# Kernel tuning notes

Measured on AMD Instinct MI355X. Metric: run time of the kernel, lower is better.

## Reference

```python
import jax, jax.numpy as jnp
import numpy as np

NUM_GROUPS = 9
POWER_P = 4.0
B = 8192

def setup_inputs() -> dict:
    key = jax.random.key(0)
    k1, k2, k3 = jax.random.split(key, 3)
    return {
        "logits_tox": jax.random.normal(k1, (B, 1), dtype=jnp.float32),
        "y_tox": jax.random.uniform(k2, (B, 1), dtype=jnp.float32),
        "y_id": jax.random.uniform(k3, (B, NUM_GROUPS), dtype=jnp.float32),
    }

def reference(logits_tox, y_tox, y_id):
    logits = logits_tox[:, 0]                      # [B]
    is_toxic = y_tox[:, 0] >= 0.5                  # [B] bool
    # D[i, j] = softplus(-(logits[i] - logits[j])) = softplus(logits[j] - logits[i])
    # row index i plays the 'pos' role, column index j plays the 'neg' role.
    D = jax.nn.softplus(logits[None, :] - logits[:, None])  # [B, B]

    in_group = (y_id >= 0.5).T                     # [G, B]
    tox = is_toxic[None, :]                        # [1, B]
    dt = logits.dtype
    sub_pos = (in_group & tox).astype(dt)          # [G, B]
    sub_neg = (in_group & ~tox).astype(dt)
    bg_pos = (~in_group & tox).astype(dt)
    bg_neg = (~in_group & ~tox).astype(dt)

    # three pair types: (sub_pos, sub_neg), (bg_pos, sub_neg), (sub_pos, bg_neg)
    pos_masks = jnp.stack([sub_pos, bg_pos, sub_pos])   # [3, G, B]
    neg_masks = jnp.stack([sub_neg, sub_neg, bg_neg])   # [3, G, B]

    num = jnp.einsum('tgi,ij,tgj->tg', pos_masks, D, neg_masks)  # [3, G]
    cnt = pos_masks.sum(-1) * neg_masks.sum(-1)                  # [3, G] n_pos*n_neg
    valid = cnt > 0                                              # pair type contributes only if both sides nonempty
    type_loss = num / jnp.maximum(cnt, 1.0)

    n_valid = valid.astype(dt).sum(0)                            # [G]
    group_loss = (type_loss * valid.astype(dt)).sum(0) / jnp.maximum(n_valid, 1.0)
    gv = (n_valid > 0).astype(dt)                                # [G] group validity
    n_groups = jnp.maximum(gv.sum(), 1.0)

    # power-mean aggregation (power_p = 4 > 1)
    mean_p = (jnp.power(group_loss, POWER_P) * gv).sum() / n_groups
    loss = jnp.power(mean_p, 1.0 / POWER_P)
    return jnp.where(gv.sum() > 0, loss, jnp.array(0.0, dt))
```

## Files before the change

kernel.cpp:

```cpp
#include <hip/hip_runtime.h>
#include <math.h>

#define NG 9
#define NBI 8
#define NBJ 128
#define NBLK (NBI * NBJ)
#define NS 3
#define IMAX 1024
#define LOG2E 1.4426950408889634f
#define LN2   0.6931471805599453f
#define ROWS 47

__global__ __launch_bounds__(256, 4) void k_fused(
    const float* __restrict__ logits, const float* __restrict__ ytox,
    const float* __restrict__ yid, int B, float* __restrict__ part) {

    __shared__ float iL[IMAX];
    __shared__ int   iM[IMAX];
    __shared__ float jLl[256];
    __shared__ int   jMl[256];
    __shared__ int   swcnt[4], swoff[4], sbase;
    __shared__ int   scT[4][NG], scN[4][NG];
    __shared__ float red[4][27];
    __shared__ float acc[27];

    const int tid = threadIdx.x, lane = tid & 63, wave = tid >> 6;
    const int blk = blockIdx.x;
    const int bi = blk & (NBI - 1), bj = blk >> 3;
    const int IRAW = (B + NBI - 1) / NBI;
    const int JRAW = (B + NBJ - 1) / NBJ;
    const unsigned long long lt = (1ull << lane) - 1ull;

    if (tid < 4 * NG) { scT[tid / NG][tid % NG] = 0; scN[tid / NG][tid % NG] = 0; }
    if (tid == 0) sbase = 0;
    if (tid < 27) acc[tid] = 0.f;
    __syncthreads();

    const int ibase0 = bi * IRAW;
    for (int r0 = 0; r0 < IRAW; r0 += 256) {
        const int row = ibase0 + r0 + tid;
        const bool valid = (r0 + tid < IRAW) && (row < B);
        float l = 0.f; bool tox = false; int m = 0;
        if (valid) {
            l = logits[row] * LOG2E;
            tox = ytox[row] >= 0.5f;
#pragma unroll
            for (int g = 0; g < NG; ++g)
                if (yid[row * NG + g] >= 0.5f) m |= 1 << g;
        }
        const unsigned long long bal = __ballot(tox);
        const int pos = __popcll(bal & lt);
        if (lane == 0) swcnt[wave] = __popcll(bal);
#pragma unroll
        for (int g = 0; g < NG; ++g) {
            const unsigned long long bg = __ballot(tox && ((m >> g) & 1));
            if (lane == 0) scT[wave][g] += __popcll(bg);
        }
        __syncthreads();
        if (tid == 0) {
            int b = sbase;
#pragma unroll
            for (int w = 0; w < 4; ++w) { swoff[w] = b; b += swcnt[w]; }
            sbase = b;
        }
        __syncthreads();
        if (tox) { const int p = swoff[wave] + pos; iL[p] = l; iM[p] = m; }
    }
    __syncthreads();
    const int nIloc = sbase;
    __syncthreads();
    if (tid == 0) sbase = 0;

    const int jbase0 = bj * JRAW;
    for (int r0 = 0; r0 < JRAW; r0 += 256) {
        const int row = jbase0 + r0 + tid;
        const bool valid = (r0 + tid < JRAW) && (row < B);
        float l = 0.f; bool nt = false; int m = 0;
        if (valid) {
            l = logits[row] * LOG2E;
            nt = ytox[row] < 0.5f;
#pragma unroll
            for (int g = 0; g < NG; ++g)
                if (yid[row * NG + g] >= 0.5f) m |= 1 << g;
        }
        const unsigned long long bal = __ballot(nt);
        const int pos = __popcll(bal & lt);
        if (lane == 0) swcnt[wave] = __popcll(bal);
#pragma unroll
        for (int g = 0; g < NG; ++g) {
            const unsigned long long bg = __ballot(nt && ((m >> g) & 1));
            if (lane == 0) scN[wave][g] += __popcll(bg);
        }
        __syncthreads();
        if (tid == 0) {
            int b = sbase;
#pragma unroll
            for (int w = 0; w < 4; ++w) { swoff[w] = b; b += swcnt[w]; }
            sbase = b;
        }
        __syncthreads();
        if (nt) { const int p = swoff[wave] + pos; jLl[p] = l; jMl[p] = m; }
    }
    __syncthreads();
    const int nJloc = sbase;

    const int ngroups = (nIloc + NS * 256 - 1) / (NS * 256);
    for (int grp = 0; grp < ngroups; ++grp) {
        float li[NS]; int mi[NS]; float Ra[NS]; float Rg[NS][NG];
#pragma unroll
        for (int u = 0; u < NS; ++u) {
            const int k = (grp * NS + u) * 256 + tid;
            const bool a = k < nIloc;
            li[u] = a ? iL[k] : 1e30f;
            mi[u] = a ? iM[k] : 0;
            Ra[u] = 0.f;
#pragma unroll
            for (int g = 0; g < NG; ++g) Rg[u][g] = 0.f;
        }
#pragma unroll 4
        for (int k = 0; k < nJloc; ++k) {
            const float lj = jLl[k];
            const int mj = __builtin_amdgcn_readfirstlane(jMl[k]);
            float s[NS];
#pragma unroll
            for (int u = 0; u < NS; ++u) {
                s[u] = __builtin_amdgcn_logf(1.f + __builtin_amdgcn_exp2f(lj - li[u]));
                Ra[u] += s[u];
            }
#pragma unroll
            for (int g = 0; g < NG; ++g) {
                const float bg = ((mj >> g) & 1) ? 1.f : 0.f;
#pragma unroll
                for (int u = 0; u < NS; ++u) Rg[u][g] = fmaf(bg, s[u], Rg[u][g]);
            }
        }
#pragma unroll
        for (int g = 0; g < NG; ++g) {
            float x0 = 0.f, x1 = 0.f, x2 = 0.f;
#pragma unroll
            for (int u = 0; u < NS; ++u) {
                const bool ing = (mi[u] >> g) & 1;
                x0 += ing ? Rg[u][g] : 0.f;
                x1 += ing ? 0.f : Rg[u][g];
                x2 += ing ? (Ra[u] - Rg[u][g]) : 0.f;
            }
#pragma unroll
            for (int off = 32; off > 0; off >>= 1) {
                x0 += __shfl_xor(x0, off, 64);
                x1 += __shfl_xor(x1, off, 64);
                x2 += __shfl_xor(x2, off, 64);
            }
            if (lane == 0) {
                red[wave][g] = x0; red[wave][NG + g] = x1; red[wave][2 * NG + g] = x2;
            }
        }
        __syncthreads();
        if (tid < 27) acc[tid] += red[0][tid] + red[1][tid] + red[2][tid] + red[3][tid];
        __syncthreads();
    }

    if (tid < 27) part[tid * NBLK + blk] = acc[tid];
    if (tid >= 32 && tid < 32 + NG) {
        const int g = tid - 32;
        part[(27 + g) * NBLK + blk] = (bj == 0)
            ? (float)(scT[0][g] + scT[1][g] + scT[2][g] + scT[3][g]) : 0.f;
    }
    if (tid == 41) part[36 * NBLK + blk] = (bj == 0) ? (float)nIloc : 0.f;
    if (tid >= 64 && tid < 64 + NG) {
        const int g = tid - 64;
        part[(37 + g) * NBLK + blk] = (bi == 0)
            ? (float)(scN[0][g] + scN[1][g] + scN[2][g] + scN[3][g]) : 0.f;
    }
    if (tid == 73) part[46 * NBLK + blk] = (bi == 0) ? (float)nJloc : 0.f;
}

__global__ __launch_bounds__(256) void k_final(
    const float* __restrict__ part, float* __restrict__ out) {
    __shared__ float fin[27];
    __shared__ float finC[20];
    const int tid = threadIdx.x, lane = tid & 63, wave = tid >> 6;

    for (int r = wave; r < 27; r += 4) {
        float s = 0.f;
#pragma unroll
        for (int q = 0; q < NBLK / 64; ++q) s += part[r * NBLK + (q << 6) + lane];
#pragma unroll
        for (int off = 32; off > 0; off >>= 1) s += __shfl_xor(s, off, 64);
        if (lane == 0) fin[r] = s * LN2;
    }
    for (int r = 27 + wave; r < ROWS; r += 4) {
        float s = 0.f;
#pragma unroll
        for (int q = 0; q < NBLK / 64; ++q) s += part[r * NBLK + (q << 6) + lane];
#pragma unroll
        for (int off = 32; off > 0; off >>= 1) s += __shfl_xor(s, off, 64);
        if (lane == 0) finC[r - 27] = s;
    }
    __syncthreads();
    if (tid == 0) {
        const long long nT64 = (long long)(finC[9] + 0.5f);
        const long long nN64 = (long long)(finC[19] + 0.5f);
        double accd = 0.0; int ngv = 0;
        for (int g = 0; g < NG; ++g) {
            const long long cT = (long long)(finC[g] + 0.5f);
            const long long cN = (long long)(finC[10 + g] + 0.5f);
            const long long c0 = cT * cN;
            const long long c1 = (nT64 - cT) * cN;
            const long long c2 = cT * (nN64 - cN);
            const double t0 = (double)fin[g]          / (double)(c0 > 0 ? c0 : 1);
            const double t1 = (double)fin[NG + g]     / (double)(c1 > 0 ? c1 : 1);
            const double t2 = (double)fin[2 * NG + g] / (double)(c2 > 0 ? c2 : 1);
            const int nv = (c0 > 0) + (c1 > 0) + (c2 > 0);
            const double gl = ((c0 > 0 ? t0 : 0.0) + (c1 > 0 ? t1 : 0.0) +
                               (c2 > 0 ? t2 : 0.0)) / (double)(nv > 0 ? nv : 1);
            if (nv > 0) { const double g2 = gl * gl; accd += g2 * g2; ++ngv; }
        }
        const double mp = accd / (double)(ngv > 0 ? ngv : 1);
        const double loss = sqrt(sqrt(mp));
        out[0] = (float)(ngv > 0 ? loss : 0.0);
    }
}

extern "C" void kernel_launch(void* const* d_in, const int* in_sizes, int n_in,
                              void* d_out, int out_size, void* d_ws, size_t ws_size,
                              hipStream_t stream) {
    const float* logits = (const float*)d_in[0];
    const float* ytox   = (const float*)d_in[1];
    const float* yid    = (const float*)d_in[2];
    const int B = in_sizes[0];
    float* part = (float*)d_ws;

    k_fused<<<dim3(NBLK), dim3(256), 0, stream>>>(logits, ytox, yid, B, part);
    k_final<<<dim3(1), dim3(256), 0, stream>>>(part, (float*)d_out);
}
```

Before: 94.80 us.

## Drop i-side LDS compaction and load toxic rows directly into registers

Removes the shared-memory compaction pass for toxic rows. Each thread now loads its i-rows straight from global memory and masks non-toxic rows with a sentinel logit, with the toxic and group counts computed by ballots in the same pass. The block grid is rebalanced to 16x64 with two slots per thread. j entries are packed into float2 in LDS, and the final reduction kernel uses 512 threads. The aim is to remove the prologue's barriers and LDS traffic, but without compaction roughly half the softplus evaluations land on masked-out rows, and each block handles more j rows.

```diff
diff --git a/kernel.cpp b/kernel.cpp
--- a/kernel.cpp
+++ b/kernel.cpp
@@ -2,74 +2,37 @@
 #include <math.h>
 
 #define NG 9
-#define NBI 8
-#define NBJ 128
+#define NBI 16
+#define NBJ 64
 #define NBLK (NBI * NBJ)
-#define NS 3
-#define IMAX 1024
+#define NS 2
+#define JCAP 256
 #define LOG2E 1.4426950408889634f
 #define LN2   0.6931471805599453f
 #define ROWS 47
 
-__global__ __launch_bounds__(256, 4) void k_fused(
+__global__ __launch_bounds__(256, 4) void k_main(
     const float* __restrict__ logits, const float* __restrict__ ytox,
     const float* __restrict__ yid, int B, float* __restrict__ part) {
 
-    __shared__ float iL[IMAX];
-    __shared__ int   iM[IMAX];
-    __shared__ float jLl[256];
-    __shared__ int   jMl[256];
+    __shared__ float2 jS[JCAP];
     __shared__ int   swcnt[4], swoff[4], sbase;
-    __shared__ int   scT[4][NG], scN[4][NG];
+    __shared__ int   scT[4][NG], scN[4][NG], scI[4];
     __shared__ float red[4][27];
     __shared__ float acc[27];
 
     const int tid = threadIdx.x, lane = tid & 63, wave = tid >> 6;
     const int blk = blockIdx.x;
-    const int bi = blk & (NBI - 1), bj = blk >> 3;
+    const int bi = blk & (NBI - 1), bj = blk >> 4;
     const int IRAW = (B + NBI - 1) / NBI;
     const int JRAW = (B + NBJ - 1) / NBJ;
     const unsigned long long lt = (1ull << lane) - 1ull;
 
     if (tid < 4 * NG) { scT[tid / NG][tid % NG] = 0; scN[tid / NG][tid % NG] = 0; }
+    if (tid < 4) scI[tid] = 0;
     if (tid == 0) sbase = 0;
     if (tid < 27) acc[tid] = 0.f;
     __syncthreads();
-
-    const int ibase0 = bi * IRAW;
-    for (int r0 = 0; r0 < IRAW; r0 += 256) {
-        const int row = ibase0 + r0 + tid;
-        const bool valid = (r0 + tid < IRAW) && (row < B);
-        float l = 0.f; bool tox = false; int m = 0;
-        if (valid) {
-            l = logits[row] * LOG2E;
-            tox = ytox[row] >= 0.5f;
-#pragma unroll
-            for (int g = 0; g < NG; ++g)
-                if (yid[row * NG + g] >= 0.5f) m |= 1 << g;
-        }
-        const unsigned long long bal = __ballot(tox);
-        const int pos = __popcll(bal & lt);
-        if (lane == 0) swcnt[wave] = __popcll(bal);
-#pragma unroll
-        for (int g = 0; g < NG; ++g) {
-            const unsigned long long bg = __ballot(tox && ((m >> g) & 1));
-            if (lane == 0) scT[wave][g] += __popcll(bg);
-        }
-        __syncthreads();
-        if (tid == 0) {
-            int b = sbase;
-#pragma unroll
-            for (int w = 0; w < 4; ++w) { swoff[w] = b; b += swcnt[w]; }
-            sbase = b;
-        }
-        __syncthreads();
-        if (tox) { const int p = swoff[wave] + pos; iL[p] = l; iM[p] = m; }
-    }
-    __syncthreads();
-    const int nIloc = sbase;
-    __syncthreads();
-    if (tid == 0) sbase = 0;
 
     const int jbase0 = bj * JRAW;
     for (int r0 = 0; r0 < JRAW; r0 += 256) {
@@ -99,28 +62,51 @@
             sbase = b;
         }
         __syncthreads();
-        if (nt) { const int p = swoff[wave] + pos; jLl[p] = l; jMl[p] = m; }
+        if (nt) jS[swoff[wave] + pos] = make_float2(l, __int_as_float(m));
     }
     __syncthreads();
     const int nJloc = sbase;
 
-    const int ngroups = (nIloc + NS * 256 - 1) / (NS * 256);
+    const int ibase0 = bi * IRAW;
+    const int islots = (IRAW + 255) >> 8;
+    const int ngroups = (islots + NS - 1) / NS;
+
     for (int grp = 0; grp < ngroups; ++grp) {
         float li[NS]; int mi[NS]; float Ra[NS]; float Rg[NS][NG];
 #pragma unroll
         for (int u = 0; u < NS; ++u) {
             const int k = (grp * NS + u) * 256 + tid;
-            const bool a = k < nIloc;
-            li[u] = a ? iL[k] : 1e30f;
-            mi[u] = a ? iM[k] : 0;
+            const int row = ibase0 + k;
+            const bool valid = (k < IRAW) && (row < B);
+            float l = 0.f; bool tox = false; int m = 0;
+            if (valid) {
+                l = logits[row] * LOG2E;
+                tox = ytox[row] >= 0.5f;
+#pragma unroll
+                for (int g = 0; g < NG; ++g)
+                    if (yid[row * NG + g] >= 0.5f) m |= 1 << g;
+            }
+            li[u] = tox ? l : 1e30f;
+            mi[u] = tox ? m : 0;
             Ra[u] = 0.f;
 #pragma unroll
             for (int g = 0; g < NG; ++g) Rg[u][g] = 0.f;
-        }
+            if (bj == 0) {
+                const unsigned long long bt = __ballot(tox);
+                if (lane == 0) scI[wave] += __popcll(bt);
+#pragma unroll
+                for (int g = 0; g < NG; ++g) {
+                    const unsigned long long bg = __ballot(tox && ((m >> g) & 1));
+                    if (lane == 0) scT[wave][g] += __popcll(bg);
+                }
+            }
+        }
+
 #pragma unroll 4
         for (int k = 0; k < nJloc; ++k) {
-            const float lj = jLl[k];
-            const int mj = __builtin_amdgcn_readfirstlane(jMl[k]);
+            const float2 jv = jS[k];
+            const float lj = jv.x;
+            const int mj = __builtin_amdgcn_readfirstlane(__float_as_int(jv.y));
             float s[NS];
 #pragma unroll
             for (int u = 0; u < NS; ++u) {
@@ -134,6 +120,7 @@
                 for (int u = 0; u < NS; ++u) Rg[u][g] = fmaf(bg, s[u], Rg[u][g]);
             }
         }
+
 #pragma unroll
         for (int g = 0; g < NG; ++g) {
             float x0 = 0.f, x1 = 0.f, x2 = 0.f;
@@ -165,7 +152,8 @@
         part[(27 + g) * NBLK + blk] = (bj == 0)
             ? (float)(scT[0][g] + scT[1][g] + scT[2][g] + scT[3][g]) : 0.f;
     }
-    if (tid == 41) part[36 * NBLK + blk] = (bj == 0) ? (float)nIloc : 0.f;
+    if (tid == 41) part[36 * NBLK + blk] = (bj == 0)
+        ? (float)(scI[0] + scI[1] + scI[2] + scI[3]) : 0.f;
     if (tid >= 64 && tid < 64 + NG) {
         const int g = tid - 64;
         part[(37 + g) * NBLK + blk] = (bi == 0)
@@ -174,13 +162,13 @@
     if (tid == 73) part[46 * NBLK + blk] = (bi == 0) ? (float)nJloc : 0.f;
 }
 
-__global__ __launch_bounds__(256) void k_final(
+__global__ __launch_bounds__(512) void k_final(
     const float* __restrict__ part, float* __restrict__ out) {
     __shared__ float fin[27];
     __shared__ float finC[20];
     const int tid = threadIdx.x, lane = tid & 63, wave = tid >> 6;
 
-    for (int r = wave; r < 27; r += 4) {
+    for (int r = wave; r < 27; r += 8) {
         float s = 0.f;
 #pragma unroll
         for (int q = 0; q < NBLK / 64; ++q) s += part[r * NBLK + (q << 6) + lane];
@@ -188,7 +176,7 @@
         for (int off = 32; off > 0; off >>= 1) s += __shfl_xor(s, off, 64);
         if (lane == 0) fin[r] = s * LN2;
     }
-    for (int r = 27 + wave; r < ROWS; r += 4) {
+    for (int r = 27 + wave; r < ROWS; r += 8) {
         float s = 0.f;
 #pragma unroll
         for (int q = 0; q < NBLK / 64; ++q) s += part[r * NBLK + (q << 6) + lane];
@@ -230,6 +218,6 @@
     const int B = in_sizes[0];
     float* part = (float*)d_ws;
 
-    k_fused<<<dim3(NBLK), dim3(256), 0, stream>>>(logits, ytox, yid, B, part);
-    k_final<<<dim3(1), dim3(256), 0, stream>>>(part, (float*)d_out);
+    k_main<<<dim3(NBLK), dim3(256), 0, stream>>>(logits, ytox, yid, B, part);
+    k_final<<<dim3(1), dim3(512), 0, stream>>>(part, (float*)d_out);
 }
```

Result: no change. 95.66 us (+0.9%).
